# Performance work log

Measured on AMD Instinct MI355X. Metric: run time of the kernel, lower is better.

## Reference

```python
import jax, jax.numpy as jnp
import numpy as np

KROT = 8
DIM = 4096
GROUP = 128
N = 16384  # tokens (batch*seq)


def setup_inputs() -> dict:
    key = jax.random.key(0)
    k1, k2, k3 = jax.random.split(key, 3)
    x = jax.random.normal(k1, (N, DIM), dtype=jnp.float16)
    theta = (jax.random.normal(k2, (KROT, DIM // 2)) * 0.5).astype(jnp.float16)
    # pairs: per rotation layer, a permutation of [0, GROUP) tiled across groups
    # (matches torch.randperm(group_size).repeat(num_groups) in the module).
    rng = np.random.default_rng(0)
    single = np.stack([rng.permutation(GROUP) for _ in range(KROT)]).astype(np.int32)  # (KROT, GROUP)
    pairs = jnp.asarray(np.tile(single, (1, DIM // GROUP)))  # (KROT, DIM)
    channel_scales = jax.random.uniform(k3, (1, DIM), minval=0.5, maxval=1.5).astype(jnp.float16)
    return {"x": x, "pairs": pairs, "theta": theta,
            "channel_scales": channel_scales, "group_size": GROUP}


def reference(x, pairs, theta, channel_scales, group_size):
    """Pairwise Givens rotations + per-channel scaling.

    For each rotation layer k, channels are grouped into blocks of
    `group_size`; consecutive entries (pairs[k, 2i], pairs[k, 2i+1]) within a
    group define a rotated channel pair with angle theta[k, i].
    """
    krot, dim = pairs.shape
    # global channel index = group offset + within-group index from `pairs`
    offs = (jnp.arange(dim) // group_size) * group_size            # (dim,)
    gidx = pairs + offs[None, :]                                   # (krot, dim)
    a_idx = gidx[:, 0::2]                                          # (krot, dim//2)
    b_idx = gidx[:, 1::2]                                          # (krot, dim//2)

    for k in range(krot):  # krot is a small fixed constant (8)
        t = theta[k].astype(jnp.float32)
        c = jnp.cos(t).astype(x.dtype)                             # (dim//2,)
        s = jnp.sin(t).astype(x.dtype)
        xa = x[:, a_idx[k]]                                        # (N, dim//2)
        xb = x[:, b_idx[k]]
        x = x.at[:, a_idx[k]].set(c * xa - s * xb)
        x = x.at[:, b_idx[k]].set(s * xa + c * xb)
    return x * channel_scales
```

## Files before the change

### kernel.cpp

```cpp
#include <hip/hip_runtime.h>
#include <hip/hip_fp16.h>


typedef unsigned int uint32;
typedef unsigned short ushort;

#define DIM    4096
#define GROUP  128
#define KROT   8
#define NGROUP 32
#define TPAD   (GROUP + 1)

typedef float    f32x4 __attribute__((ext_vector_type(4)));
typedef _Float16 f16x8 __attribute__((ext_vector_type(8)));

union Uh { uint4 u; f16x8 h; };

__device__ __forceinline__ float bf16_to_f(ushort u) {
    union { uint32 i; float f; } v; v.i = ((uint32)u) << 16; return v.f;
}
__device__ __forceinline__ ushort f_to_bf16(float f) {
    union { float f; uint32 i; } v; v.f = f;
    uint32 x = v.i;
    return (ushort)((x + 0x7fffu + ((x >> 16) & 1u)) >> 16);
}
__device__ __forceinline__ float fp16_to_f(ushort u) {
    __half h = __ushort_as_half(u); return __half2float(h);
}
__device__ __forceinline__ ushort f_to_fp16(float f) {
    return __half_as_ushort(__float2half_rn(f));
}
__device__ __forceinline__ float bcast_f(float x, int lane) {
    return __uint_as_float(__builtin_amdgcn_readlane(__float_as_uint(x), lane));
}
__device__ __forceinline__ ushort h_bits(_Float16 h) {
    union { _Float16 f; ushort s; } v; v.f = h; return v.s;
}

__global__ __launch_bounds__(256) void detect_dtype(const uint32* __restrict__ scw,
                                                    int* __restrict__ flag) {
    __shared__ int cbf[256], cfp16[256];
    int b = 0, h = 0;
    for (int i = threadIdx.x; i < 2048; i += 256) {
        uint32 lo = scw[i] & 0xffffu;
        b += (lo >= 0x3F00u && lo <= 0x3FC0u);
        h += (lo >= 0x3800u && lo <= 0x3E00u);
    }
    cbf[threadIdx.x] = b; cfp16[threadIdx.x] = h;
    __syncthreads();
    for (int s = 128; s > 0; s >>= 1) {
        if (threadIdx.x < s) { cbf[threadIdx.x] += cbf[threadIdx.x + s];
                               cfp16[threadIdx.x] += cfp16[threadIdx.x + s]; }
        __syncthreads();
    }
    if (threadIdx.x == 0)
        *flag = (cbf[0] > 1024) ? 1 : ((cfp16[0] > 1024) ? 2 : 0);
}

__global__ __launch_bounds__(256) void compose_M(
    const int*  __restrict__ pairs,
    const void* __restrict__ thetav,
    const void* __restrict__ scalesv,
    ushort*     __restrict__ Mth,
    ushort*     __restrict__ Mtl,
    const int*  __restrict__ flagp)
{
    __shared__ float tile[64][TPAD];
    const int dt = *flagp;
    if (dt != 0) return;
    const int g    = blockIdx.x >> 1;
    const int half = blockIdx.x & 1;
    const int r0   = half * 64;
    const int tid  = threadIdx.x;
    const int l    = tid & 63;
    const int w    = tid >> 6;
    const int pmine = w * 16 + (l & 15);

    int Ak[KROT], Bk[KROT]; float Ck[KROT], Sk[KROT];
    #pragma unroll
    for (int k = 0; k < KROT; ++k) {
        Ak[k] = pairs[k * DIM + g * GROUP + 2 * pmine];
        Bk[k] = pairs[k * DIM + g * GROUP + 2 * pmine + 1];
        float th = ((const float*)thetav)[k * (DIM / 2) + g * (GROUP / 2) + pmine];
        Ck[k] = __builtin_cosf(th); Sk[k] = __builtin_sinf(th);
    }
    for (int idx = tid; idx < 64 * GROUP; idx += 256) {
        int r = idx >> 7, c = idx & 127;
        tile[r][c] = (r0 + r == c) ? 1.0f : 0.0f;
    }
    __syncthreads();
    #pragma unroll
    for (int k = 0; k < KROT; ++k) {
        #pragma unroll
        for (int pp = 0; pp < 16; ++pp) {
            int   a = __builtin_amdgcn_readlane(Ak[k], pp);
            int   b = __builtin_amdgcn_readlane(Bk[k], pp);
            float c = bcast_f(Ck[k], pp);
            float s = bcast_f(Sk[k], pp);
            float xa = tile[l][a], xb = tile[l][b];
            tile[l][a] = c * xa - s * xb;
            tile[l][b] = s * xa + c * xb;
        }
        __syncthreads();
    }
    for (int it = 0; it < 4; ++it) {
        int idx = it * 256 + tid;
        int j = idx >> 3, cc = idx & 7;
        float sj = ((const float*)scalesv)[g * GROUP + j];
        union { ushort s[8]; uint4 u; } ph, pl;
        #pragma unroll
        for (int e = 0; e < 8; ++e) {
            float m = tile[cc * 8 + e][j] * sj;
            _Float16 hh = (_Float16)m;
            float r = m - (float)hh;
            ph.s[e] = h_bits(hh);
            pl.s[e] = h_bits((_Float16)r);
        }
        size_t off = (size_t)g * (GROUP * GROUP) + (size_t)j * GROUP + r0 + cc * 8;
        *(uint4*)(Mth + off) = ph.u;
        *(uint4*)(Mtl + off) = pl.u;
    }
}

__global__ __launch_bounds__(256, 1) void rotate_gemm(
    const void* __restrict__ Xv,
    const ushort* __restrict__ Mth,
    const ushort* __restrict__ Mtl,
    void* __restrict__ Outv,
    const int* __restrict__ flagp,
    const int* __restrict__ pairs,
    const void* __restrict__ thetav,
    const void* __restrict__ scalesv,
    int nrows)
{
    __shared__ float tile[64][TPAD];
    __shared__ float scl[GROUP];
    const int dt  = *flagp;
    const int bid = blockIdx.x;
    const int g   = bid & 31;
    const int sub = bid >> 5;
    const int ntiles = nrows >> 6;
    const int tid = threadIdx.x;
    const int l   = tid & 63;
    const int w   = tid >> 6;
    const int lr  = l & 15;
    const int q   = l >> 4;

    if (dt == 0) {
        const int wr = w >> 1, wc = w & 1;
        const float* Xg = (const float*)Xv;
        float*       Og = (float*)Outv;

        uint4 BH[4][4], BL[4][4];
        #pragma unroll
        for (int nf = 0; nf < 4; ++nf) {
            #pragma unroll
            for (int kk = 0; kk < 4; ++kk) {
                size_t off = (size_t)g * (GROUP * GROUP)
                           + (size_t)(wc * 64 + nf * 16 + lr) * GROUP
                           + kk * 32 + q * 8;
                BH[nf][kk] = *(const uint4*)(Mth + off);
                BL[nf][kk] = *(const uint4*)(Mtl + off);
            }
        }

        uint4 A0[2][4][2], A1[2][4][2];

        auto loadA = [&](uint4 (&A)[2][4][2], int t) {
            const int R0 = t * 64;
            #pragma unroll
            for (int mf = 0; mf < 2; ++mf) {
                #pragma unroll
                for (int kk = 0; kk < 4; ++kk) {
                    const float* p = Xg + (size_t)(R0 + wr * 32 + mf * 16 + lr) * DIM
                                        + g * GROUP + kk * 32 + q * 8;
                    A[mf][kk][0] = *(const uint4*)p;
                    A[mf][kk][1] = *(const uint4*)(p + 4);
                }
            }
        };

        auto computeStore = [&](const uint4 (&A)[2][4][2], int t) {
            f16x8 ah[2][4], al[2][4];
            #pragma unroll
            for (int mf = 0; mf < 2; ++mf) {
                #pragma unroll
                for (int kk = 0; kk < 4; ++kk) {
                    f16x8 hv, lv;
                    #pragma unroll
                    for (int h4 = 0; h4 < 2; ++h4) {
                        union { uint4 u; float f[4]; } uu; uu.u = A[mf][kk][h4];
                        #pragma unroll
                        for (int e = 0; e < 4; ++e) {
                            float x = uu.f[e];
                            _Float16 hh = (_Float16)x;
                            float r = x - (float)hh;
                            hv[h4 * 4 + e] = hh;
                            lv[h4 * 4 + e] = (_Float16)r;
                        }
                    }
                    ah[mf][kk] = hv; al[mf][kk] = lv;
                }
            }
            f32x4 acc[2][4];
            #pragma unroll
            for (int mf = 0; mf < 2; ++mf)
                #pragma unroll
                for (int nf = 0; nf < 4; ++nf)
                    acc[mf][nf] = (f32x4)0.0f;
            #pragma unroll
            for (int kk = 0; kk < 4; ++kk) {
                #pragma unroll
                for (int nf = 0; nf < 4; ++nf) {
                    Uh bh, bl; bh.u = BH[nf][kk]; bl.u = BL[nf][kk];
                    #pragma unroll
                    for (int mf = 0; mf < 2; ++mf) {
                        acc[mf][nf] = __builtin_amdgcn_mfma_f32_16x16x32_f16(
                            ah[mf][kk], bh.h, acc[mf][nf], 0, 0, 0);
                        acc[mf][nf] = __builtin_amdgcn_mfma_f32_16x16x32_f16(
                            al[mf][kk], bh.h, acc[mf][nf], 0, 0, 0);
                        acc[mf][nf] = __builtin_amdgcn_mfma_f32_16x16x32_f16(
                            ah[mf][kk], bl.h, acc[mf][nf], 0, 0, 0);
                    }
                }
            }
            const int R0 = t * 64;
            #pragma unroll
            for (int mf = 0; mf < 2; ++mf) {
                #pragma unroll
                for (int nf = 0; nf < 4; ++nf) {
                    float* bp = Og + (size_t)(R0 + wr * 32 + mf * 16 + q * 4) * DIM
                                   + g * GROUP + wc * 64 + nf * 16 + lr;
                    #pragma unroll
                    for (int j = 0; j < 4; ++j)
                        __builtin_nontemporal_store(acc[mf][nf][j], bp + (size_t)j * DIM);
                }
            }
        };

        int t = sub;
        if (t < ntiles) {
            loadA(A0, t);
            while (true) {
                int t1 = t + 8;
                if (t1 < ntiles) loadA(A1, t1);
                computeStore(A0, t);
                if (t1 >= ntiles) break;
                int t2 = t1 + 8;
                if (t2 < ntiles) loadA(A0, t2);
                computeStore(A1, t1);
                if (t2 >= ntiles) break;
                t = t2;
            }
        }
        return;
    }

    {
        const int pmine = w * 16 + (l & 15);
        if (tid < GROUP) {
            int c = g * GROUP + tid;
            scl[tid] = (dt == 1) ? bf16_to_f(((const ushort*)scalesv)[c])
                                 : fp16_to_f(((const ushort*)scalesv)[c]);
        }
        int Ak[KROT], Bk[KROT]; float Ck[KROT], Sk[KROT];
        #pragma unroll
        for (int k = 0; k < KROT; ++k) {
            Ak[k] = pairs[k * DIM + g * GROUP + 2 * pmine];
            Bk[k] = pairs[k * DIM + g * GROUP + 2 * pmine + 1];
            int ti = k * (DIM / 2) + g * (GROUP / 2) + pmine;
            float th = (dt == 1) ? bf16_to_f(((const ushort*)thetav)[ti])
                                 : fp16_to_f(((const ushort*)thetav)[ti]);
            Ck[k] = __builtin_cosf(th); Sk[k] = __builtin_sinf(th);
        }
        for (int t = sub; t < ntiles; t += 8) {
            const int row0 = t * 64;
            const uint4* X4 = (const uint4*)Xv;
            for (int i = tid; i < 64 * 16; i += 256) {
                int r = i >> 4, c8 = i & 15;
                uint4 wv = X4[(size_t)(row0 + r) * (DIM / 8) + g * (GROUP / 8) + c8];
                uint32 ws[4] = { wv.x, wv.y, wv.z, wv.w };
                #pragma unroll
                for (int h2 = 0; h2 < 4; ++h2) {
                    ushort lo = (ushort)(ws[h2] & 0xffffu);
                    ushort hi = (ushort)(ws[h2] >> 16);
                    tile[r][c8 * 8 + 2 * h2]     = (dt == 1) ? bf16_to_f(lo) : fp16_to_f(lo);
                    tile[r][c8 * 8 + 2 * h2 + 1] = (dt == 1) ? bf16_to_f(hi) : fp16_to_f(hi);
                }
            }
            __syncthreads();
            #pragma unroll
            for (int k = 0; k < KROT; ++k) {
                #pragma unroll
                for (int pp = 0; pp < 16; ++pp) {
                    int   a = __builtin_amdgcn_readlane(Ak[k], pp);
                    int   b = __builtin_amdgcn_readlane(Bk[k], pp);
                    float c = bcast_f(Ck[k], pp);
                    float s = bcast_f(Sk[k], pp);
                    float xa = tile[l][a], xb = tile[l][b];
                    tile[l][a] = c * xa - s * xb;
                    tile[l][b] = s * xa + c * xb;
                }
                __syncthreads();
            }
            uint4* O4 = (uint4*)Outv;
            for (int i = tid; i < 64 * 16; i += 256) {
                int r = i >> 4, c8 = i & 15;
                uint32 ws[4];
                #pragma unroll
                for (int h2 = 0; h2 < 4; ++h2) {
                    float lo = tile[r][c8 * 8 + 2 * h2]     * scl[c8 * 8 + 2 * h2];
                    float hi = tile[r][c8 * 8 + 2 * h2 + 1] * scl[c8 * 8 + 2 * h2 + 1];
                    ushort ulo = (dt == 1) ? f_to_bf16(lo) : f_to_fp16(lo);
                    ushort uhi = (dt == 1) ? f_to_bf16(hi) : f_to_fp16(hi);
                    ws[h2] = (uint32)ulo | ((uint32)uhi << 16);
                }
                uint4 wv; wv.x = ws[0]; wv.y = ws[1]; wv.z = ws[2]; wv.w = ws[3];
                O4[(size_t)(row0 + r) * (DIM / 8) + g * (GROUP / 8) + c8] = wv;
            }
            __syncthreads();
        }
    }
}

__global__ __launch_bounds__(256) void rotate_direct(
    const void* __restrict__ Xv,
    const int*  __restrict__ pairs,
    const void* __restrict__ thetav,
    const void* __restrict__ scalesv,
    void* __restrict__ Outv,
    const int* __restrict__ flagp, int defflag)
{
    __shared__ float tile[64][TPAD];
    __shared__ float scl[GROUP];
    const int g    = blockIdx.x;
    const int row0 = blockIdx.y * 64;
    const int tid  = threadIdx.x;
    const int dt   = flagp ? *flagp : defflag;
    const int l    = tid & 63;
    const int w    = tid >> 6;
    const int pmine = w * 16 + (l & 15);

    if (tid < GROUP) {
        int c = g * GROUP + tid;
        scl[tid] = (dt == 1) ? bf16_to_f(((const ushort*)scalesv)[c])
                 : (dt == 2) ? fp16_to_f(((const ushort*)scalesv)[c])
                 : ((const float*)scalesv)[c];
    }
    int Ak[KROT], Bk[KROT]; float Ck[KROT], Sk[KROT];
    #pragma unroll
    for (int k = 0; k < KROT; ++k) {
        Ak[k] = pairs[k * DIM + g * GROUP + 2 * pmine];
        Bk[k] = pairs[k * DIM + g * GROUP + 2 * pmine + 1];
        int ti = k * (DIM / 2) + g * (GROUP / 2) + pmine;
        float th = (dt == 1) ? bf16_to_f(((const ushort*)thetav)[ti])
                 : (dt == 2) ? fp16_to_f(((const ushort*)thetav)[ti])
                 : ((const float*)thetav)[ti];
        Ck[k] = __builtin_cosf(th);
        Sk[k] = __builtin_sinf(th);
    }
    if (dt == 0) {
        const float4* X4 = (const float4*)Xv;
        for (int i = tid; i < 64 * 32; i += 256) {
            int r = i >> 5, c4 = i & 31;
            float4 v = X4[(size_t)(row0 + r) * (DIM / 4) + g * (GROUP / 4) + c4];
            tile[r][c4 * 4 + 0] = v.x; tile[r][c4 * 4 + 1] = v.y;
            tile[r][c4 * 4 + 2] = v.z; tile[r][c4 * 4 + 3] = v.w;
        }
    } else {
        const uint4* X4 = (const uint4*)Xv;
        for (int i = tid; i < 64 * 16; i += 256) {
            int r = i >> 4, c8 = i & 15;
            uint4 wv = X4[(size_t)(row0 + r) * (DIM / 8) + g * (GROUP / 8) + c8];
            uint32 ws[4] = { wv.x, wv.y, wv.z, wv.w };
            #pragma unroll
            for (int h2 = 0; h2 < 4; ++h2) {
                ushort lo = (ushort)(ws[h2] & 0xffffu);
                ushort hi = (ushort)(ws[h2] >> 16);
                tile[r][c8 * 8 + 2 * h2]     = (dt == 1) ? bf16_to_f(lo) : fp16_to_f(lo);
                tile[r][c8 * 8 + 2 * h2 + 1] = (dt == 1) ? bf16_to_f(hi) : fp16_to_f(hi);
            }
        }
    }
    __syncthreads();
    #pragma unroll
    for (int k = 0; k < KROT; ++k) {
        #pragma unroll
        for (int pp = 0; pp < 16; ++pp) {
            int   a = __builtin_amdgcn_readlane(Ak[k], pp);
            int   b = __builtin_amdgcn_readlane(Bk[k], pp);
            float c = bcast_f(Ck[k], pp);
            float s = bcast_f(Sk[k], pp);
            float xa = tile[l][a], xb = tile[l][b];
            tile[l][a] = c * xa - s * xb;
            tile[l][b] = s * xa + c * xb;
        }
        __syncthreads();
    }
    if (dt == 0) {
        float4* O4 = (float4*)Outv;
        for (int i = tid; i < 64 * 32; i += 256) {
            int r = i >> 5, c4 = i & 31;
            float4 v;
            v.x = tile[r][c4 * 4 + 0] * scl[c4 * 4 + 0];
            v.y = tile[r][c4 * 4 + 1] * scl[c4 * 4 + 1];
            v.z = tile[r][c4 * 4 + 2] * scl[c4 * 4 + 2];
            v.w = tile[r][c4 * 4 + 3] * scl[c4 * 4 + 3];
            O4[(size_t)(row0 + r) * (DIM / 4) + g * (GROUP / 4) + c4] = v;
        }
    } else {
        uint4* O4 = (uint4*)Outv;
        for (int i = tid; i < 64 * 16; i += 256) {
            int r = i >> 4, c8 = i & 15;
            uint32 ws[4];
            #pragma unroll
            for (int h2 = 0; h2 < 4; ++h2) {
                float lo = tile[r][c8 * 8 + 2 * h2]     * scl[c8 * 8 + 2 * h2];
                float hi = tile[r][c8 * 8 + 2 * h2 + 1] * scl[c8 * 8 + 2 * h2 + 1];
                ushort ulo = (dt == 1) ? f_to_bf16(lo) : f_to_fp16(lo);
                ushort uhi = (dt == 1) ? f_to_bf16(hi) : f_to_fp16(hi);
                ws[h2] = (uint32)ulo | ((uint32)uhi << 16);
            }
            uint4 wv; wv.x = ws[0]; wv.y = ws[1]; wv.z = ws[2]; wv.w = ws[3];
            O4[(size_t)(row0 + r) * (DIM / 8) + g * (GROUP / 8) + c8] = wv;
        }
    }
}

extern "C" void kernel_launch(void* const* d_in, const int* in_sizes, int n_in,
                              void* d_out, int out_size, void* d_ws, size_t ws_size,
                              hipStream_t stream) {
    const void* x      = d_in[0];
    const int*  pairs  = (const int*)d_in[1];
    const void* theta  = d_in[2];
    const void* scales = d_in[3];

    const int nrows = in_sizes[0] / DIM;
    const int nrowtiles = nrows / 64;

    const size_t MSZ  = (size_t)NGROUP * GROUP * GROUP * 2;
    const size_t NEED = 64 + 2 * MSZ;

    if (d_ws != nullptr && ws_size >= NEED) {
        int*    flag = (int*)d_ws;
        ushort* Mth  = (ushort*)((char*)d_ws + 64);
        ushort* Mtl  = (ushort*)((char*)d_ws + 64 + MSZ);
        detect_dtype<<<1, 256, 0, stream>>>((const uint32*)scales, flag);
        compose_M<<<64, 256, 0, stream>>>(pairs, theta, scales, Mth, Mtl, flag);
        rotate_gemm<<<256, 256, 0, stream>>>(
            x, Mth, Mtl, d_out, flag, pairs, theta, scales, nrows);
    } else if (d_ws != nullptr && ws_size >= sizeof(int)) {
        int* flag = (int*)d_ws;
        detect_dtype<<<1, 256, 0, stream>>>((const uint32*)scales, flag);
        rotate_direct<<<dim3(NGROUP, nrowtiles), 256, 0, stream>>>(
            x, pairs, theta, scales, d_out, flag, 0);
    } else {
        rotate_direct<<<dim3(NGROUP, nrowtiles), 256, 0, stream>>>(
            x, pairs, theta, scales, d_out, nullptr, 0);
    }
}
```

Measured before the change: 472.7 us.

## Raise rotate_gemm occupancy with 4x grid and simplify fp32 GEMM pipeline

Launches rotate_gemm with 1024 blocks instead of 256, changes the tile stride from 8 to 32 to match, and allows two blocks per CU through launch bounds. This is meant to hide global-memory latency with more resident waves. The fp32 path swaps its double-buffered loads for a single register buffer that prefetches the next tile before the stores. It also drops the low-part split of the input operand, which cuts MFMA work and registers but lowers precision. With fp16 inputs only the grid and stride change affects the fp16 rotation path that actually runs.

New measurement: 478.5 us. Within noise of the previous version (+1.2%).

```diff
diff --git a/kernel.cpp b/kernel.cpp
--- a/kernel.cpp
+++ b/kernel.cpp
@@ -35,6 +35,15 @@
 }
 __device__ __forceinline__ ushort h_bits(_Float16 h) {
     union { _Float16 f; ushort s; } v; v.f = h; return v.s;
+}
+__device__ __forceinline__ f16x8 cvt8(uint4 a0, uint4 a1) {
+    union { uint4 u; float f[4]; } x, y; x.u = a0; y.u = a1;
+    f16x8 r;
+    r[0] = (_Float16)x.f[0]; r[1] = (_Float16)x.f[1];
+    r[2] = (_Float16)x.f[2]; r[3] = (_Float16)x.f[3];
+    r[4] = (_Float16)y.f[0]; r[5] = (_Float16)y.f[1];
+    r[6] = (_Float16)y.f[2]; r[7] = (_Float16)y.f[3];
+    return r;
 }
 
 __global__ __launch_bounds__(256) void detect_dtype(const uint32* __restrict__ scw,
@@ -122,7 +131,7 @@
     }
 }
 
-__global__ __launch_bounds__(256, 1) void rotate_gemm(
+__global__ __launch_bounds__(256, 2) void rotate_gemm(
     const void* __restrict__ Xv,
     const ushort* __restrict__ Mth,
     const ushort* __restrict__ Mtl,
@@ -164,93 +173,66 @@
             }
         }
 
-        uint4 A0[2][4][2], A1[2][4][2];
-
-        auto loadA = [&](uint4 (&A)[2][4][2], int t) {
+        uint4 Araw[2][4][2];
+
+        auto loadA = [&](int t) {
             const int R0 = t * 64;
             #pragma unroll
             for (int mf = 0; mf < 2; ++mf) {
+                const float* p = Xg + (size_t)(R0 + wr * 32 + mf * 16 + lr) * DIM
+                                    + g * GROUP + q * 8;
                 #pragma unroll
                 for (int kk = 0; kk < 4; ++kk) {
-                    const float* p = Xg + (size_t)(R0 + wr * 32 + mf * 16 + lr) * DIM
-                                        + g * GROUP + kk * 32 + q * 8;
-                    A[mf][kk][0] = *(const uint4*)p;
-                    A[mf][kk][1] = *(const uint4*)(p + 4);
-                }
-            }
-        };
-
-        auto computeStore = [&](const uint4 (&A)[2][4][2], int t) {
-            f16x8 ah[2][4], al[2][4];
-            #pragma unroll
-            for (int mf = 0; mf < 2; ++mf) {
-                #pragma unroll
-                for (int kk = 0; kk < 4; ++kk) {
-                    f16x8 hv, lv;
-                    #pragma unroll
-                    for (int h4 = 0; h4 < 2; ++h4) {
-                        union { uint4 u; float f[4]; } uu; uu.u = A[mf][kk][h4];
-                        #pragma unroll
-                        for (int e = 0; e < 4; ++e) {
-                            float x = uu.f[e];
-                            _Float16 hh = (_Float16)x;
-                            float r = x - (float)hh;
-                            hv[h4 * 4 + e] = hh;
-                            lv[h4 * 4 + e] = (_Float16)r;
-                        }
-                    }
-                    ah[mf][kk] = hv; al[mf][kk] = lv;
-                }
-            }
-            f32x4 acc[2][4];
-            #pragma unroll
-            for (int mf = 0; mf < 2; ++mf)
-                #pragma unroll
-                for (int nf = 0; nf < 4; ++nf)
-                    acc[mf][nf] = (f32x4)0.0f;
-            #pragma unroll
-            for (int kk = 0; kk < 4; ++kk) {
-                #pragma unroll
-                for (int nf = 0; nf < 4; ++nf) {
-                    Uh bh, bl; bh.u = BH[nf][kk]; bl.u = BL[nf][kk];
-                    #pragma unroll
-                    for (int mf = 0; mf < 2; ++mf) {
-                        acc[mf][nf] = __builtin_amdgcn_mfma_f32_16x16x32_f16(
-                            ah[mf][kk], bh.h, acc[mf][nf], 0, 0, 0);
-                        acc[mf][nf] = __builtin_amdgcn_mfma_f32_16x16x32_f16(
-                            al[mf][kk], bh.h, acc[mf][nf], 0, 0, 0);
-                        acc[mf][nf] = __builtin_amdgcn_mfma_f32_16x16x32_f16(
-                            ah[mf][kk], bl.h, acc[mf][nf], 0, 0, 0);
-                    }
-                }
-            }
-            const int R0 = t * 64;
-            #pragma unroll
-            for (int mf = 0; mf < 2; ++mf) {
-                #pragma unroll
-                for (int nf = 0; nf < 4; ++nf) {
-                    float* bp = Og + (size_t)(R0 + wr * 32 + mf * 16 + q * 4) * DIM
-                                   + g * GROUP + wc * 64 + nf * 16 + lr;
-                    #pragma unroll
-                    for (int j = 0; j < 4; ++j)
-                        __builtin_nontemporal_store(acc[mf][nf][j], bp + (size_t)j * DIM);
+                    Araw[mf][kk][0] = *(const uint4*)(p + kk * 32);
+                    Araw[mf][kk][1] = *(const uint4*)(p + kk * 32 + 4);
                 }
             }
         };
 
         int t = sub;
         if (t < ntiles) {
-            loadA(A0, t);
+            loadA(t);
             while (true) {
-                int t1 = t + 8;
-                if (t1 < ntiles) loadA(A1, t1);
-                computeStore(A0, t);
-                if (t1 >= ntiles) break;
-                int t2 = t1 + 8;
-                if (t2 < ntiles) loadA(A0, t2);
-                computeStore(A1, t1);
-                if (t2 >= ntiles) break;
-                t = t2;
+                f32x4 acc[2][4];
+                #pragma unroll
+                for (int mf = 0; mf < 2; ++mf)
+                    #pragma unroll
+                    for (int nf = 0; nf < 4; ++nf)
+                        acc[mf][nf] = (f32x4)0.0f;
+                #pragma unroll
+                for (int kk = 0; kk < 4; ++kk) {
+                    f16x8 ah0 = cvt8(Araw[0][kk][0], Araw[0][kk][1]);
+                    f16x8 ah1 = cvt8(Araw[1][kk][0], Araw[1][kk][1]);
+                    #pragma unroll
+                    for (int nf = 0; nf < 4; ++nf) {
+                        Uh bh, bl; bh.u = BH[nf][kk]; bl.u = BL[nf][kk];
+                        acc[0][nf] = __builtin_amdgcn_mfma_f32_16x16x32_f16(
+                            ah0, bh.h, acc[0][nf], 0, 0, 0);
+                        acc[0][nf] = __builtin_amdgcn_mfma_f32_16x16x32_f16(
+                            ah0, bl.h, acc[0][nf], 0, 0, 0);
+                        acc[1][nf] = __builtin_amdgcn_mfma_f32_16x16x32_f16(
+                            ah1, bh.h, acc[1][nf], 0, 0, 0);
+                        acc[1][nf] = __builtin_amdgcn_mfma_f32_16x16x32_f16(
+                            ah1, bl.h, acc[1][nf], 0, 0, 0);
+                    }
+                }
+                const int tn = t + 32;
+                if (tn < ntiles) loadA(tn);
+                const int R0 = t * 64;
+                #pragma unroll
+                for (int mf = 0; mf < 2; ++mf) {
+                    #pragma unroll
+                    for (int nf = 0; nf < 4; ++nf) {
+                        float* bp = Og + (size_t)(R0 + wr * 32 + mf * 16 + q * 4) * DIM
+                                       + g * GROUP + wc * 64 + nf * 16 + lr;
+                        #pragma unroll
+                        for (int j = 0; j < 4; ++j)
+                            __builtin_nontemporal_store(acc[mf][nf][j],
+                                                        bp + (size_t)j * DIM);
+                    }
+                }
+                if (tn >= ntiles) break;
+                t = tn;
             }
         }
         return;
@@ -273,7 +255,7 @@
                                  : fp16_to_f(((const ushort*)thetav)[ti]);
             Ck[k] = __builtin_cosf(th); Sk[k] = __builtin_sinf(th);
         }
-        for (int t = sub; t < ntiles; t += 8) {
+        for (int t = sub; t < ntiles; t += 32) {
             const int row0 = t * 64;
             const uint4* X4 = (const uint4*)Xv;
             for (int i = tid; i < 64 * 16; i += 256) {
@@ -447,7 +429,7 @@
         ushort* Mtl  = (ushort*)((char*)d_ws + 64 + MSZ);
         detect_dtype<<<1, 256, 0, stream>>>((const uint32*)scales, flag);
         compose_M<<<64, 256, 0, stream>>>(pairs, theta, scales, Mth, Mtl, flag);
-        rotate_gemm<<<256, 256, 0, stream>>>(
+        rotate_gemm<<<1024, 256, 0, stream>>>(
             x, Mth, Mtl, d_out, flag, pairs, theta, scales, nrows);
     } else if (d_ws != nullptr && ws_size >= sizeof(int)) {
         int* flag = (int*)d_ws;
```
